# Kernel optimization log

Hardware: AMD Instinct MI355X
Metric: run time of the kernel (lower is better)

Reference implementation:

```python
import jax, jax.numpy as jnp
import numpy as np
from jax import lax

DIM, HEADS, BS, TOPK, WIN = 256, 8, 8, 4, 7
HID = 2 * DIM  # DBFFN ffn_expansion_factor=2
B, H, W = 2, 56, 56


def _lin(x, w, b=None):
    # torch Linear: y = x @ W.T + b, W is [out, in]
    y = jnp.einsum('...c,oc->...o', x, w)
    return y if b is None else y + b


def _ln(x, w, b, eps=1e-6):
    mu = jnp.mean(x, -1, keepdims=True)
    var = jnp.mean((x - mu) ** 2, -1, keepdims=True)
    return (x - mu) * lax.rsqrt(var + eps) * w + b


def _mha(Q, K, V, wq_w, wq_b, wk_w, wk_b, wv_w, wv_b, p_w, p_b):
    # standard cross MHA: Q [B,Nq,C], K/V [B,Nk,C]
    Bq, Nq, C = Q.shape
    h, d = HEADS, C // HEADS
    scale = d ** -0.5
    q = _lin(Q, wq_w, wq_b).reshape(Bq, Nq, h, d)
    k = _lin(K, wk_w, wk_b).reshape(Bq, -1, h, d)
    v = _lin(V, wv_w, wv_b).reshape(Bq, -1, h, d)
    attn = jax.nn.softmax(jnp.einsum('bnhd,bmhd->bhnm', q, k) * scale, axis=-1)
    out = jnp.einsum('bhnm,bmhd->bnhd', attn, v).reshape(Bq, Nq, C)
    return _lin(out, p_w, p_b)


def setup_inputs() -> dict:
    key = jax.random.key(0)
    ks = jax.random.split(key, 16)
    s = 0.02
    C = DIM
    inp = {
        'x': jax.random.normal(ks[0], (B, C, H, W), jnp.float32),
        'pos_w': jax.random.normal(ks[1], (C, 1, 3, 3), jnp.float32) * s,
        'pos_b': jnp.zeros((C,), jnp.float32),
        'n1_w': jnp.ones((C,), jnp.float32), 'n1_b': jnp.zeros((C,), jnp.float32),
        'n2_w': jnp.ones((C,), jnp.float32), 'n2_b': jnp.zeros((C,), jnp.float32),
        'wq_w': jax.random.normal(ks[2], (3, C, C), jnp.float32) * s,
        'wq_b': jnp.zeros((3, C), jnp.float32),
        'wk_w': jax.random.normal(ks[3], (3, C, C), jnp.float32) * s,
        'wk_b': jnp.zeros((3, C), jnp.float32),
        'wv_w': jax.random.normal(ks[4], (3, C, C), jnp.float32) * s,
        'wv_b': jnp.zeros((3, C), jnp.float32),
        'pj_w': jax.random.normal(ks[5], (3, C, C), jnp.float32) * s,
        'pj_b': jnp.zeros((3, C), jnp.float32),
        # block scorer
        's1_w': jax.random.normal(ks[6], (C // 2, C), jnp.float32) * s,
        's1_b': jnp.zeros((C // 2,), jnp.float32),
        's2_w': jax.random.normal(ks[7], (1, C // 2), jnp.float32) * s,
        's2_b': jnp.zeros((1,), jnp.float32),
        # gating: per-token softmax weights over 3 branches
        'g_w': jax.random.normal(ks[8], (3, C), jnp.float32) * s,
        'g_b': jnp.zeros((3,), jnp.float32),
        # DBFFN (gated dconv FFN, bias=False): in-proj C->2*HID, dw 3x3, out-proj HID->C
        'pin_w': jax.random.normal(ks[9], (2 * HID, C), jnp.float32) * s,
        'dw_w': jax.random.normal(ks[10], (3, 3, 1, 2 * HID), jnp.float32) * s,
        'pout_w': jax.random.normal(ks[11], (C, HID), jnp.float32) * s,
    }
    return inp


def _forward(x, pos_w, pos_b, n1_w, n1_b, n2_w, n2_b, wq_w, wq_b, wk_w, wk_b,
             wv_w, wv_b, pj_w, pj_b, s1_w, s1_b, s2_w, s2_b, g_w, g_b,
             pin_w, dw_w, pout_w):
    Bx, C, Hx, Wx = x.shape
    # depthwise positional conv
    pos = lax.conv_general_dilated(x, pos_w, (1, 1), 'SAME',
                                   dimension_numbers=('NCHW', 'OIHW', 'NCHW'),
                                   feature_group_count=C)
    x = x + pos + pos_b[None, :, None, None] * 0 + pos_b[None, :, None, None]
    feat = jnp.transpose(x, (0, 2, 3, 1))  # NHWC
    Nq = Hx * Wx
    Q = feat.reshape(Bx, Nq, C)
    # block means
    nH, nW = Hx // BS, Wx // BS
    nB = nH * nW
    blk = feat.reshape(Bx, nH, BS, nW, BS, C).transpose(0, 1, 3, 2, 4, 5)
    blk = blk.reshape(Bx, nB, BS * BS, C).mean(axis=2)  # [B,nB,C]
    # block scores + top-k selection
    hsc = jax.nn.gelu(_lin(blk, s1_w, s1_b), approximate=False)
    scores = _lin(hsc, s2_w, s2_b)[..., 0]  # [B,nB]
    topk = min(TOPK, nB)
    _, idx = lax.top_k(scores, topk)
    K_sel = jnp.take_along_axis(blk, idx[:, :, None], axis=1)  # [B,topk,C]
    # compressed + selected branches
    y_cmp = _mha(Q, blk, blk, wq_w[0], wq_b[0], wk_w[0], wk_b[0], wv_w[0], wv_b[0], pj_w[0], pj_b[0])
    y_sel = _mha(Q, K_sel, K_sel, wq_w[1], wq_b[1], wk_w[1], wk_b[1], wv_w[1], wv_b[1], pj_w[1], pj_b[1])
    # local window branch (replicate-pad + unfold == shifted slices)
    pad = WIN // 2
    padded = jnp.pad(feat, ((0, 0), (pad, pad), (pad, pad), (0, 0)), mode='edge')
    patches = jnp.stack([padded[:, dy:dy + Hx, dx:dx + Wx, :]
                         for dy in range(WIN) for dx in range(WIN)], axis=3)
    patches = patches.reshape(Bx, Nq, WIN * WIN, C)  # [B,Nq,49,C]
    h, d = HEADS, C // HEADS
    scale = d ** -0.5
    q = _lin(Q, wq_w[2], wq_b[2]).reshape(Bx, Nq, h, d)
    k = _lin(patches, wk_w[2], wk_b[2]).reshape(Bx, Nq, WIN * WIN, h, d)
    v = _lin(patches, wv_w[2], wv_b[2]).reshape(Bx, Nq, WIN * WIN, h, d)
    attn = jax.nn.softmax(jnp.einsum('bnhd,bnwhd->bnhw', q, k) * scale, axis=-1)
    y_win = jnp.einsum('bnhw,bnwhd->bnhd', attn, v).reshape(Bx, Nq, C)
    y_win = _lin(y_win, pj_w[2], pj_b[2])
    # gated fusion + residual
    qn = _ln(Q, n1_w, n1_b)
    g = jax.nn.softmax(_lin(qn, g_w, g_b), axis=-1)  # [B,Nq,3]
    y = g[..., 0:1] * y_cmp + g[..., 1:2] * y_sel + g[..., 2:3] * y_win + Q
    ym = y.reshape(Bx, Hx, Wx, C)
    # DBFFN: gated depthwise-conv FFN (bias-free)
    t = _lin(ym, pin_w)  # [B,H,W,2*HID]
    t = lax.conv_general_dilated(t, dw_w, (1, 1), 'SAME',
                                 dimension_numbers=('NHWC', 'HWIO', 'NHWC'),
                                 feature_group_count=2 * HID)
    x1, x2 = jnp.split(t, 2, axis=-1)
    mlp = _lin(jax.nn.gelu(x1, approximate=False) * x2, pout_w)
    ym = _ln(ym + mlp, n2_w, n2_b)
    return jnp.transpose(ym, (0, 3, 1, 2))  # NCHW


def reference(x, pos_w, pos_b, n1_w, n1_b, n2_w, n2_b, wq_w, wq_b, wk_w, wk_b,
              wv_w, wv_b, pj_w, pj_b, s1_w, s1_b, s2_w, s2_b, g_w, g_b,
              pin_w, dw_w, pout_w):
    return _forward(x, pos_w, pos_b, n1_w, n1_b, n2_w, n2_b, wq_w, wq_b, wk_w,
                    wk_b, wv_w, wv_b, pj_w, pj_b, s1_w, s1_b, s2_w, s2_b,
                    g_w, g_b, pin_w, dw_w, pout_w)
```

## Files before the change

### kernel.cpp

```cpp
#include <hip/hip_runtime.h>

#define BATCH 2
#define CDIM 256
#define HEADS 8
#define HD 32
#define HH 56
#define WW 56
#define NQ 3136
#define NTOK 6272
#define NB 49
#define NTOPK 4
#define HID2 1024
#define HIDM 512
#define QSTRH 1280
#define ASTR 768

typedef short bf16x8 __attribute__((ext_vector_type(8)));
typedef float f32x4 __attribute__((ext_vector_type(4)));
typedef _Float16 h2 __attribute__((ext_vector_type(2)));
typedef _Float16 h4 __attribute__((ext_vector_type(4)));
struct __align__(16) h2x4 { h2 x, y, z, w; };

__device__ __forceinline__ float gelu_exact(float x) {
    return 0.5f * x * (1.f + erff(x * 0.70710678118654752f));
}

__device__ __forceinline__ short f2bf(float f) {
    union { float f; unsigned u; } v; v.f = f;
    unsigned r = v.u + 0x7FFFu + ((v.u >> 16) & 1u);
    return (short)(r >> 16);
}

__device__ __forceinline__ float fdot2h(h2 a, h2 b, float c) {
#if __has_builtin(__builtin_amdgcn_fdot2)
    return __builtin_amdgcn_fdot2(a, b, c, false);
#else
    return c + (float)a[0] * (float)b[0] + (float)a[1] * (float)b[1];
#endif
}

__device__ __forceinline__ void gld16(const void* gsrc, void* ldst) {
    __builtin_amdgcn_global_load_lds(
        (const __attribute__((address_space(1))) void*)gsrc,
        (__attribute__((address_space(3))) void*)ldst, 16, 0, 0);
}

__global__ __launch_bounds__(256) void k_init(
        const float* __restrict__ x, float* __restrict__ xT,
        const float* __restrict__ wq_w, const float* __restrict__ wk_w,
        const float* __restrict__ wv_w, const float* __restrict__ wq_b,
        const float* __restrict__ wk_b, const float* __restrict__ wv_b,
        const float* __restrict__ pj_w, const float* __restrict__ pin_w,
        const float* __restrict__ pout_w,
        short* __restrict__ Wc1, short* __restrict__ Wpj,
        short* __restrict__ Wpin, short* __restrict__ Wpout,
        float* __restrict__ bias1, float* __restrict__ Wkv0,
        float* __restrict__ bkv0, float* __restrict__ Wkv1,
        float* __restrict__ bkv1) {
    __shared__ float t[64][65];
    int bid = blockIdx.x;
    int tid = threadIdx.x;
    if (bid < 392) {
        int p0 = (bid % 49) * 64;
        int c0 = ((bid / 49) & 3) * 64;
        int b  = bid / 196;
        int pi = tid & 63, cj = tid >> 6;
        #pragma unroll
        for (int j = 0; j < 16; j++) {
            int c = cj * 16 + j;
            t[c][pi] = x[((size_t)(b * CDIM + c0 + c)) * NQ + p0 + pi];
        }
        __syncthreads();
        int ci = tid & 63, pj = tid >> 6;
        #pragma unroll
        for (int j = 0; j < 16; j++) {
            int p = pj * 16 + j;
            xT[((size_t)(b * NQ + p0 + p)) * CDIM + c0 + ci] = t[ci][p];
        }
        return;
    }
    int i = (bid - 392) * 256 + tid;
    if (i < 327680) {
        int r = i >> 8, k = i & 255, seg = r >> 8, n = r & 255;
        float v;
        if (seg == 0)      v = wq_w[n * 256 + k];
        else if (seg == 1) v = wq_w[65536 + n * 256 + k];
        else if (seg == 2) v = wq_w[131072 + n * 256 + k];
        else if (seg == 3) v = wk_w[131072 + n * 256 + k];
        else               v = wv_w[131072 + n * 256 + k];
        Wc1[i] = f2bf(v);
    } else if (i < 524288) {
        int j = i - 327680;
        int n = j / 768, tt = j % 768, br = tt >> 8, k = tt & 255;
        Wpj[j] = f2bf(pj_w[br * 65536 + n * 256 + k]);
    } else if (i < 786432) {
        int j = i - 524288;
        int r = j >> 8, k = j & 255;
        int o = (r & 3) * 256 + (r >> 2);
        Wpin[j] = f2bf(pin_w[o * 256 + k]);
    } else if (i < 917504) {
        int j = i - 786432;
        Wpout[j] = f2bf(pout_w[j]);
    } else if (i < 1048576) {
        int j = i - 917504;
        int r = j >> 8, k = j & 255;
        Wkv0[j] = (r < 256) ? wk_w[r * 256 + k] : wv_w[(r - 256) * 256 + k];
    } else if (i < 1179648) {
        int j = i - 1048576;
        int r = j >> 8, k = j & 255;
        Wkv1[j] = (r < 256) ? wk_w[65536 + r * 256 + k] : wv_w[65536 + (r - 256) * 256 + k];
    } else if (i < 1180928) {
        int j = i - 1179648;
        float v;
        if (j < 768)       v = wq_b[j];
        else if (j < 1024) v = wk_b[512 + (j - 768)];
        else               v = wv_b[512 + (j - 1024)];
        bias1[j] = v;
    } else if (i < 1181440) {
        int j = i - 1180928;
        bkv0[j] = (j < 256) ? wk_b[j] : wv_b[j - 256];
    } else if (i < 1181952) {
        int j = i - 1181440;
        bkv1[j] = (j < 256) ? wk_b[256 + j] : wv_b[j];
    }
}

__global__ __launch_bounds__(256) void k_posgates(
        const float* __restrict__ xT, const float* __restrict__ pw,
        const float* __restrict__ pb, const float* __restrict__ n1w,
        const float* __restrict__ n1b, const float* __restrict__ gw,
        const float* __restrict__ gb, float* __restrict__ feat,
        float* __restrict__ g, short* __restrict__ featb) {
    int wvid = threadIdx.x >> 6;
    int lane = threadIdx.x & 63;
    int c4 = lane * 4;
    float pwv[4][9];
    #pragma unroll
    for (int j = 0; j < 4; j++)
        #pragma unroll
        for (int i = 0; i < 9; i++) pwv[j][i] = pw[(c4 + j) * 9 + i];
    float4 pbv = *(const float4*)(pb + c4);
    float4 w1 = *(const float4*)(n1w + c4);
    float4 b1 = *(const float4*)(n1b + c4);
    float4 gw0 = *(const float4*)(gw + c4);
    float4 gw1 = *(const float4*)(gw + CDIM + c4);
    float4 gw2 = *(const float4*)(gw + 2 * CDIM + c4);
    float gb0 = gb[0], gb1 = gb[1], gb2 = gb[2];
    int tbase = blockIdx.x * 16 + wvid * 4;
    for (int t = 0; t < 4; t++) {
        int bn = tbase + t;
        int b = bn / NQ, n = bn % NQ;
        int y = n / WW, x = n % WW;
        const float* xb = xT + (size_t)b * NQ * CDIM;
        float4 a = *(const float4*)(xb + (size_t)n * CDIM + c4);
        float acc0 = a.x + pbv.x, acc1 = a.y + pbv.y;
        float acc2 = a.z + pbv.z, acc3 = a.w + pbv.w;
        #pragma unroll
        for (int dy = 0; dy < 3; dy++) {
            int yy = y + dy - 1;
            if (yy < 0 || yy >= HH) continue;
            #pragma unroll
            for (int dx = 0; dx < 3; dx++) {
                int xx = x + dx - 1;
                if (xx < 0 || xx >= WW) continue;
                float4 v = *(const float4*)(xb + ((size_t)(yy * WW + xx)) * CDIM + c4);
                int wi = dy * 3 + dx;
                acc0 += v.x * pwv[0][wi];
                acc1 += v.y * pwv[1][wi];
                acc2 += v.z * pwv[2][wi];
                acc3 += v.w * pwv[3][wi];
            }
        }
        *(float4*)(feat + (size_t)bn * CDIM + c4) = make_float4(acc0, acc1, acc2, acc3);
        short4 fb;
        fb.x = f2bf(acc0); fb.y = f2bf(acc1); fb.z = f2bf(acc2); fb.w = f2bf(acc3);
        *(short4*)(featb + (size_t)bn * CDIM + c4) = fb;
        float s = acc0 + acc1 + acc2 + acc3;
        #pragma unroll
        for (int off = 32; off > 0; off >>= 1) s += __shfl_xor(s, off);
        float mu = s * (1.f / CDIM);
        float d0 = acc0 - mu, d1 = acc1 - mu, d2 = acc2 - mu, d3 = acc3 - mu;
        float ss = d0 * d0 + d1 * d1 + d2 * d2 + d3 * d3;
        #pragma unroll
        for (int off = 32; off > 0; off >>= 1) ss += __shfl_xor(ss, off);
        float rstd = rsqrtf(ss * (1.f / CDIM) + 1e-6f);
        float q0 = d0 * rstd * w1.x + b1.x;
        float q1 = d1 * rstd * w1.y + b1.y;
        float q2 = d2 * rstd * w1.z + b1.z;
        float q3 = d3 * rstd * w1.w + b1.w;
        float p0 = q0 * gw0.x + q1 * gw0.y + q2 * gw0.z + q3 * gw0.w;
        float p1 = q0 * gw1.x + q1 * gw1.y + q2 * gw1.z + q3 * gw1.w;
        float p2 = q0 * gw2.x + q1 * gw2.y + q2 * gw2.z + q3 * gw2.w;
        #pragma unroll
        for (int off = 32; off > 0; off >>= 1) {
            p0 += __shfl_xor(p0, off);
            p1 += __shfl_xor(p1, off);
            p2 += __shfl_xor(p2, off);
        }
        if (lane == 0) {
            float l0 = p0 + gb0, l1 = p1 + gb1, l2 = p2 + gb2;
            float m3 = fmaxf(l0, fmaxf(l1, l2));
            float e0 = __expf(l0 - m3), e1 = __expf(l1 - m3), e2 = __expf(l2 - m3);
            float inv = 1.f / (e0 + e1 + e2);
            g[bn * 3 + 0] = e0 * inv;
            g[bn * 3 + 1] = e1 * inv;
            g[bn * 3 + 2] = e2 * inv;
        }
    }
}

__global__ __launch_bounds__(256) void k_blkscore(
        const float* __restrict__ feat, const float* __restrict__ s1w,
        const float* __restrict__ s1b, const float* __restrict__ s2w,
        const float* __restrict__ s2b, float* __restrict__ blk,
        float* __restrict__ scores) {
    __shared__ float sblk[256];
    __shared__ float red[128];
    int gid = blockIdx.x;
    int b = gid / NB, bid = gid % NB;
    int by = bid / 7, bx = bid % 7;
    int c = threadIdx.x;
    float s = 0.f;
    for (int iy = 0; iy < 8; iy++)
        for (int ix = 0; ix < 8; ix++) {
            int y = by * 8 + iy, xx = bx * 8 + ix;
            s += feat[((size_t)(b * NQ + y * WW + xx)) * CDIM + c];
        }
    s *= (1.f / 64.f);
    blk[(size_t)gid * CDIM + c] = s;
    sblk[c] = s;
    __syncthreads();
    if (c < 128) {
        const float* wrow = s1w + (size_t)c * CDIM;
        float acc = s1b[c];
        for (int k = 0; k < CDIM; k++) acc += sblk[k] * wrow[k];
        red[c] = gelu_exact(acc) * s2w[c];
    }
    __syncthreads();
    #pragma unroll
    for (int st = 64; st > 0; st >>= 1) {
        if (c < st) red[c] += red[c + st];
        __syncthreads();
    }
    if (c == 0) scores[gid] = red[0] + s2b[0];
}

__global__ __launch_bounds__(256) void k_qkvkv(
        const short* __restrict__ A, const short* __restrict__ W,
        const float* __restrict__ bias, _Float16* __restrict__ C2,
        const float* __restrict__ blk, const float* __restrict__ Wkv0,
        const float* __restrict__ bkv0, _Float16* __restrict__ kvcmp,
        const float* __restrict__ scores, const float* __restrict__ Wkv1,
        const float* __restrict__ bkv1, _Float16* __restrict__ kvsel) {
    __shared__ __align__(16) char sm[27648];
    int bid = blockIdx.x;
    int tid = threadIdx.x;
    if (bid < 980) {
        const int K = 256, N = 1280;
        short (*As)[72] = (short(*)[72])sm;
        short (*Bs)[72] = (short(*)[72])(sm + 64 * 72 * 2);
        int wid = tid >> 6, lane = tid & 63;
        int wm = wid >> 1, wn = wid & 1;
        int m0 = (bid / 10) * 64, n0 = (bid % 10) * 128;
        f32x4 acc[2][4] = {};
        int ar = tid >> 2, ac = (tid & 3) * 16;
        int br = tid >> 1, bc = (tid & 1) * 32;
        int fr = lane & 15, fk = (lane >> 4) * 8;
        for (int k0 = 0; k0 < K; k0 += 64) {
            const short* ap = A + (size_t)(m0 + ar) * K + k0 + ac;
            bf16x8 a0 = *(const bf16x8*)(ap);
            bf16x8 a1 = *(const bf16x8*)(ap + 8);
            const short* wp = W + (size_t)(n0 + br) * K + k0 + bc;
            bf16x8 w0 = *(const bf16x8*)(wp);
            bf16x8 w1 = *(const bf16x8*)(wp + 8);
            bf16x8 w2 = *(const bf16x8*)(wp + 16);
            bf16x8 w3 = *(const bf16x8*)(wp + 24);
            __syncthreads();
            *(bf16x8*)&As[ar][ac] = a0;
            *(bf16x8*)&As[ar][ac + 8] = a1;
            *(bf16x8*)&Bs[br][bc] = w0;
            *(bf16x8*)&Bs[br][bc + 8] = w1;
            *(bf16x8*)&Bs[br][bc + 16] = w2;
            *(bf16x8*)&Bs[br][bc + 24] = w3;
            __syncthreads();
            #pragma unroll
            for (int kk = 0; kk < 64; kk += 32) {
                bf16x8 af[2], bf[4];
                #pragma unroll
                for (int mi = 0; mi < 2; mi++)
                    af[mi] = *(const bf16x8*)&As[wm * 32 + mi * 16 + fr][kk + fk];
                #pragma unroll
                for (int ni = 0; ni < 4; ni++)
                    bf[ni] = *(const bf16x8*)&Bs[wn * 64 + ni * 16 + fr][kk + fk];
                #pragma unroll
                for (int mi = 0; mi < 2; mi++)
                    #pragma unroll
                    for (int ni = 0; ni < 4; ni++)
                        acc[mi][ni] = __builtin_amdgcn_mfma_f32_16x16x32_bf16(
                            af[mi], bf[ni], acc[mi][ni], 0, 0, 0);
            }
        }
        int rsub = (lane >> 4) * 4;
        #pragma unroll
        for (int mi = 0; mi < 2; mi++) {
            #pragma unroll
            for (int ni = 0; ni < 4; ni++) {
                int col = n0 + wn * 64 + ni * 16 + (lane & 15);
                float bv = bias[col];
                #pragma unroll
                for (int r = 0; r < 4; r++) {
                    int row = m0 + wm * 32 + mi * 16 + rsub + r;
                    C2[(size_t)row * N + col] = (_Float16)(acc[mi][ni][r] + bv);
                }
            }
        }
    } else {
        float (*As)[68] = (float(*)[68])sm;
        float (*Ws)[68] = (float(*)[68])(sm + 16 * 68 * 4);
        float (*ssc)[NB] = (float(*)[NB])(sm + 2 * 16 * 68 * 4);
        int* sidx = (int*)(sm + 2 * 16 * 68 * 4 + 2 * NB * 4);
        int kid = bid - 980;
        int kvy = kid >> 3, kvx = kid & 7;
        const float* Wk; const float* biask; _Float16* C; int M;
        int m0;
        bool sel = (kvy == 2);
        if (!sel) { Wk = Wkv0; biask = bkv0; C = kvcmp; M = 98; m0 = kvy * 64; }
        else      { Wk = Wkv1; biask = bkv1; C = kvsel; M = 8;  m0 = 0; }
        const int N = 512, K = 256;
        const int tx = tid & 15, ty = tid >> 4;
        const int n0 = kvx * 64;
        const int lr = tid >> 2;
        const int lk = (tid & 3) * 4;
        if (sel) {
            if (tid < 2 * NB) ssc[tid / NB][tid % NB] = scores[tid];
            __syncthreads();
            if (tid < 2) {
                for (int t = 0; t < NTOPK; t++) {
                    int best = 0; float bv = -1e30f;
                    for (int m = 0; m < NB; m++)
                        if (ssc[tid][m] > bv) { bv = ssc[tid][m]; best = m; }
                    sidx[tid * 4 + t] = best; ssc[tid][best] = -1e30f;
                }
            }
            __syncthreads();
        }
        int gm = m0 + lr;
        int arow = gm;
        if (sel && gm < 8) arow = (gm >> 2) * NB + sidx[gm];
        float acc[4][4] = {};
        for (int k0 = 0; k0 < K; k0 += 16) {
            float4 av = make_float4(0.f, 0.f, 0.f, 0.f);
            if (gm < M) av = *(const float4*)(blk + (size_t)arow * K + k0 + lk);
            int gn = n0 + lr;
            float4 wv = *(const float4*)(Wk + (size_t)gn * K + k0 + lk);
            __syncthreads();
            As[lk][lr] = av.x; As[lk + 1][lr] = av.y; As[lk + 2][lr] = av.z; As[lk + 3][lr] = av.w;
            Ws[lk][lr] = wv.x; Ws[lk + 1][lr] = wv.y; Ws[lk + 2][lr] = wv.z; Ws[lk + 3][lr] = wv.w;
            __syncthreads();
            #pragma unroll
            for (int kk = 0; kk < 16; kk++) {
                const float4 a = *(const float4*)&As[kk][ty * 4];
                const float4 b = *(const float4*)&Ws[kk][tx * 4];
                acc[0][0] += a.x * b.x; acc[0][1] += a.x * b.y; acc[0][2] += a.x * b.z; acc[0][3] += a.x * b.w;
                acc[1][0] += a.y * b.x; acc[1][1] += a.y * b.y; acc[1][2] += a.y * b.z; acc[1][3] += a.y * b.w;
                acc[2][0] += a.z * b.x; acc[2][1] += a.z * b.y; acc[2][2] += a.z * b.z; acc[2][3] += a.z * b.w;
                acc[3][0] += a.w * b.x; acc[3][1] += a.w * b.y; acc[3][2] += a.w * b.z; acc[3][3] += a.w * b.w;
            }
        }
        #pragma unroll
        for (int i = 0; i < 4; i++) {
            int om = m0 + ty * 4 + i;
            if (om >= M) break;
            #pragma unroll
            for (int j = 0; j < 4; j++) {
                int gn = n0 + tx * 4 + j;
                C[(size_t)om * N + gn] = (_Float16)(acc[i][j] + biask[gn]);
            }
        }
    }
}

__global__ __launch_bounds__(256) void k_gemm64x128(
        const short* __restrict__ A, const short* __restrict__ W,
        const float* __restrict__ bias, int M, int N, int K,
        _Float16* __restrict__ C2) {
    __shared__ short As[64][72];
    __shared__ short Bs[128][72];
    int tid = threadIdx.x;
    int wid = tid >> 6, lane = tid & 63;
    int wm = wid >> 1, wn = wid & 1;
    int m0 = blockIdx.y * 64, n0 = blockIdx.x * 128;
    f32x4 acc[2][4] = {};
    int ar = tid >> 2, ac = (tid & 3) * 16;
    int br = tid >> 1, bc = (tid & 1) * 32;
    int fr = lane & 15, fk = (lane >> 4) * 8;
    for (int k0 = 0; k0 < K; k0 += 64) {
        const short* ap = A + (size_t)(m0 + ar) * K + k0 + ac;
        bf16x8 a0 = *(const bf16x8*)(ap);
        bf16x8 a1 = *(const bf16x8*)(ap + 8);
        const short* wp = W + (size_t)(n0 + br) * K + k0 + bc;
        bf16x8 w0 = *(const bf16x8*)(wp);
        bf16x8 w1 = *(const bf16x8*)(wp + 8);
        bf16x8 w2 = *(const bf16x8*)(wp + 16);
        bf16x8 w3 = *(const bf16x8*)(wp + 24);
        __syncthreads();
        *(bf16x8*)&As[ar][ac] = a0;
        *(bf16x8*)&As[ar][ac + 8] = a1;
        *(bf16x8*)&Bs[br][bc] = w0;
        *(bf16x8*)&Bs[br][bc + 8] = w1;
        *(bf16x8*)&Bs[br][bc + 16] = w2;
        *(bf16x8*)&Bs[br][bc + 24] = w3;
        __syncthreads();
        #pragma unroll
        for (int kk = 0; kk < 64; kk += 32) {
            bf16x8 af[2], bf[4];
            #pragma unroll
            for (int mi = 0; mi < 2; mi++)
                af[mi] = *(const bf16x8*)&As[wm * 32 + mi * 16 + fr][kk + fk];
            #pragma unroll
            for (int ni = 0; ni < 4; ni++)
                bf[ni] = *(const bf16x8*)&Bs[wn * 64 + ni * 16 + fr][kk + fk];
            #pragma unroll
            for (int mi = 0; mi < 2; mi++)
                #pragma unroll
                for (int ni = 0; ni < 4; ni++)
                    acc[mi][ni] = __builtin_amdgcn_mfma_f32_16x16x32_bf16(
                        af[mi], bf[ni], acc[mi][ni], 0, 0, 0);
        }
    }
    int rsub = (lane >> 4) * 4;
    #pragma unroll
    for (int mi = 0; mi < 2; mi++) {
        #pragma unroll
        for (int ni = 0; ni < 4; ni++) {
            int col = n0 + wn * 64 + ni * 16 + (lane & 15);
            float bv = bias ? bias[col] : 0.f;
            #pragma unroll
            for (int r = 0; r < 4; r++) {
                int row = m0 + wm * 32 + mi * 16 + rsub + r;
                C2[(size_t)row * N + col] = (_Float16)(acc[mi][ni][r] + bv);
            }
        }
    }
}

__global__ __launch_bounds__(256) void k_gemm64(
        const short* __restrict__ A, const short* __restrict__ W,
        const float* __restrict__ bias, float* __restrict__ C,
        int M, int N, int K,
        const float* __restrict__ resid, const float* __restrict__ g3,
        const float* __restrict__ pjb, short* __restrict__ Cb) {
    __shared__ short As[64][72];
    __shared__ short Bs[64][72];
    int tid = threadIdx.x;
    int wid = tid >> 6, lane = tid & 63;
    int wm = wid >> 1, wn = wid & 1;
    int m0 = blockIdx.y * 64, n0 = blockIdx.x * 64;
    f32x4 acc[2][2] = {};
    int ar = tid >> 2, ac = (tid & 3) * 16;
    int fr = lane & 15, fk = (lane >> 4) * 8;
    for (int k0 = 0; k0 < K; k0 += 64) {
        const short* ap = A + (size_t)(m0 + ar) * K + k0 + ac;
        bf16x8 a0 = *(const bf16x8*)(ap);
        bf16x8 a1 = *(const bf16x8*)(ap + 8);
        const short* wp = W + (size_t)(n0 + ar) * K + k0 + ac;
        bf16x8 w0 = *(const bf16x8*)(wp);
        bf16x8 w1 = *(const bf16x8*)(wp + 8);
        __syncthreads();
        *(bf16x8*)&As[ar][ac] = a0;
        *(bf16x8*)&As[ar][ac + 8] = a1;
        *(bf16x8*)&Bs[ar][ac] = w0;
        *(bf16x8*)&Bs[ar][ac + 8] = w1;
        __syncthreads();
        #pragma unroll
        for (int kk = 0; kk < 64; kk += 32) {
            bf16x8 af[2], bf[2];
            #pragma unroll
            for (int mi = 0; mi < 2; mi++)
                af[mi] = *(const bf16x8*)&As[wm * 32 + mi * 16 + fr][kk + fk];
            #pragma unroll
            for (int ni = 0; ni < 2; ni++)
                bf[ni] = *(const bf16x8*)&Bs[wn * 32 + ni * 16 + fr][kk + fk];
            #pragma unroll
            for (int mi = 0; mi < 2; mi++)
                #pragma unroll
                for (int ni = 0; ni < 2; ni++)
                    acc[mi][ni] = __builtin_amdgcn_mfma_f32_16x16x32_bf16(
                        af[mi], bf[ni], acc[mi][ni], 0, 0, 0);
        }
    }
    int rsub = (lane >> 4) * 4;
    #pragma unroll
    for (int mi = 0; mi < 2; mi++) {
        #pragma unroll
        for (int ni = 0; ni < 2; ni++) {
            int col = n0 + wn * 32 + ni * 16 + (lane & 15);
            #pragma unroll
            for (int r = 0; r < 4; r++) {
                int row = m0 + wm * 32 + mi * 16 + rsub + r;
                float v = acc[mi][ni][r];
                if (resid) {
                    v += resid[(size_t)row * N + col]
                       + g3[row * 3 + 0] * pjb[col]
                       + g3[row * 3 + 1] * pjb[256 + col]
                       + g3[row * 3 + 2] * pjb[512 + col];
                } else if (bias) {
                    v += bias[col];
                }
                C[(size_t)row * N + col] = v;
                if (Cb) Cb[(size_t)row * N + col] = f2bf(v);
            }
        }
    }
}

__global__ __launch_bounds__(256) void k_poutln(
        const short* __restrict__ G, const short* __restrict__ W,
        const float* __restrict__ ym, const float* __restrict__ n2w,
        const float* __restrict__ n2b, float* __restrict__ out) {
    __shared__ short As[32][72];
    __shared__ float redS[4][36];
    __shared__ float redQ[4][36];
    int tid = threadIdx.x;
    int wid = tid >> 6, lane = tid & 63;
    int bx = blockIdx.x;
    int b = bx / 98;
    int t0g = bx * 32;
    int p0 = (bx % 98) * 32;
    f32x4 acc[2][4] = {};
    int ar = tid >> 3, ac = (tid & 7) * 8;
    int fr = lane & 15, fk = (lane >> 4) * 8;
    const short* Wb = W + (size_t)(wid * 64) * 512;
    for (int k0 = 0; k0 < 512; k0 += 64) {
        bf16x8 a0 = *(const bf16x8*)(G + (size_t)(t0g + ar) * 512 + k0 + ac);
        __syncthreads();
        *(bf16x8*)&As[ar][ac] = a0;
        __syncthreads();
        #pragma unroll
        for (int kk = 0; kk < 64; kk += 32) {
            bf16x8 af[2], bf[4];
            #pragma unroll
            for (int mi = 0; mi < 2; mi++)
                af[mi] = *(const bf16x8*)&As[mi * 16 + fr][kk + fk];
            #pragma unroll
            for (int ni = 0; ni < 4; ni++)
                bf[ni] = *(const bf16x8*)(Wb + (size_t)(ni * 16 + fr) * 512 + k0 + kk + fk);
            #pragma unroll
            for (int mi = 0; mi < 2; mi++)
                #pragma unroll
                for (int ni = 0; ni < 4; ni++)
                    acc[mi][ni] = __builtin_amdgcn_mfma_f32_16x16x32_bf16(
                        af[mi], bf[ni], acc[mi][ni], 0, 0, 0);
        }
    }
    int rsub = (lane >> 4) * 4;
    float v[2][4][4];
    #pragma unroll
    for (int mi = 0; mi < 2; mi++)
        #pragma unroll
        for (int ni = 0; ni < 4; ni++) {
            int col = wid * 64 + ni * 16 + fr;
            #pragma unroll
            for (int r = 0; r < 4; r++) {
                int row = mi * 16 + rsub + r;
                v[mi][ni][r] = acc[mi][ni][r] + ym[(size_t)(t0g + row) * CDIM + col];
            }
        }
    #pragma unroll
    for (int mi = 0; mi < 2; mi++) {
        #pragma unroll
        for (int r = 0; r < 4; r++) {
            float s = v[mi][0][r] + v[mi][1][r] + v[mi][2][r] + v[mi][3][r];
            s += __shfl_xor(s, 1); s += __shfl_xor(s, 2);
            s += __shfl_xor(s, 4); s += __shfl_xor(s, 8);
            if (fr == 0) redS[wid][mi * 16 + rsub + r] = s;
        }
    }
    __syncthreads();
    float mu[2][4];
    #pragma unroll
    for (int mi = 0; mi < 2; mi++)
        #pragma unroll
        for (int r = 0; r < 4; r++) {
            int row = mi * 16 + rsub + r;
            mu[mi][r] = (redS[0][row] + redS[1][row] + redS[2][row] + redS[3][row])
                        * (1.f / CDIM);
        }
    #pragma unroll
    for (int mi = 0; mi < 2; mi++) {
        #pragma unroll
        for (int r = 0; r < 4; r++) {
            float m = mu[mi][r];
            float d0 = v[mi][0][r] - m, d1 = v[mi][1][r] - m;
            float d2 = v[mi][2][r] - m, d3 = v[mi][3][r] - m;
            float q = d0 * d0 + d1 * d1 + d2 * d2 + d3 * d3;
            q += __shfl_xor(q, 1); q += __shfl_xor(q, 2);
            q += __shfl_xor(q, 4); q += __shfl_xor(q, 8);
            if (fr == 0) redQ[wid][mi * 16 + rsub + r] = q;
        }
    }
    __syncthreads();
    float rstd[2][4];
    #pragma unroll
    for (int mi = 0; mi < 2; mi++)
        #pragma unroll
        for (int r = 0; r < 4; r++) {
            int row = mi * 16 + rsub + r;
            float var = (redQ[0][row] + redQ[1][row] + redQ[2][row] + redQ[3][row])
                        * (1.f / CDIM);
            rstd[mi][r] = rsqrtf(var + 1e-6f);
        }
    #pragma unroll
    for (int mi = 0; mi < 2; mi++) {
        #pragma unroll
        for (int ni = 0; ni < 4; ni++) {
            int col = wid * 64 + ni * 16 + fr;
            float wgt = n2w[col], bia = n2b[col];
            float4 o;
            o.x = (v[mi][ni][0] - mu[mi][0]) * rstd[mi][0] * wgt + bia;
            o.y = (v[mi][ni][1] - mu[mi][1]) * rstd[mi][1] * wgt + bia;
            o.z = (v[mi][ni][2] - mu[mi][2]) * rstd[mi][2] * wgt + bia;
            o.w = (v[mi][ni][3] - mu[mi][3]) * rstd[mi][3] * wgt + bia;
            *(float4*)(out + ((size_t)(b * CDIM + col)) * NQ + p0 + mi * 16 + rsub) = o;
        }
    }
}

__global__ __launch_bounds__(512) void k_attn_lds(
        const _Float16* __restrict__ bufQ, const _Float16* __restrict__ kvc,
        const _Float16* __restrict__ kvs, short* __restrict__ Acatb,
        const float* __restrict__ g) {
    __shared__ uint4 buf[100 * 32];
    int tid = threadIdx.x;
    int wid = tid >> 6;
    int lane = tid & 63;
    int l = tid & 31;
    int tk = tid >> 5;
    int dg = l & 3;
    int co = l * 8;
    const float scale = 0.17677669529663687f;

    if (blockIdx.x < 392) {
        int bid = blockIdx.x;
        int swz = (bid & 7) * 49 + (bid >> 3);
        int t0 = swz * 16;
        int tok = t0 + tk;
        int b = t0 / NQ;
        const _Float16* kb = kvc + (size_t)b * NB * 512;
        for (int p = wid * 2; p < NB + 1; p += 16) {
            int myp = p + (lane >> 5);
            if (myp > NB - 1) myp = NB - 1;
            gld16((const uint4*)(kb + (size_t)myp * 512) + (lane & 31), &buf[p * 32]);
        }
        const _Float16* qrow = bufQ + (size_t)tok * QSTRH;
        float gate0 = g[tok * 3 + 0];
        float gate1 = g[tok * 3 + 1];
        short* orow = Acatb + (size_t)tok * ASTR;
        h2x4 qv = *(const h2x4*)(qrow + co);
        __syncthreads();
        float sc[13];
        sc[12] = -1e30f;
        #pragma unroll
        for (int m = 0; m < NB; m++) {
            h2x4 kv = *(const h2x4*)&buf[m * 32 + l];
            float acc = fdot2h(qv.x, kv.x, 0.f);
            acc = fdot2h(qv.y, kv.y, acc);
            acc = fdot2h(qv.z, kv.z, acc);
            acc = fdot2h(qv.w, kv.w, acc);
            acc += __shfl_xor(acc, 1);
            acc += __shfl_xor(acc, 2);
            if ((m & 3) == dg) sc[m >> 2] = acc * scale;
        }
        float mx = sc[0];
        #pragma unroll
        for (int i = 1; i < 13; i++) mx = fmaxf(mx, sc[i]);
        mx = fmaxf(mx, __shfl_xor(mx, 1));
        mx = fmaxf(mx, __shfl_xor(mx, 2));
        float sum = 0.f;
        #pragma unroll
        for (int i = 0; i < 13; i++) { sc[i] = __expf(sc[i] - mx); sum += sc[i]; }
        sum += __shfl_xor(sum, 1);
        sum += __shfl_xor(sum, 2);
        float inv_c = 1.f / sum;
        __syncthreads();
        for (int p = wid * 2; p < NB + 1; p += 16) {
            int myp = p + (lane >> 5);
            if (myp > NB - 1) myp = NB - 1;
            gld16((const uint4*)(kb + (size_t)myp * 512 + 256) + (lane & 31), &buf[p * 32]);
        }
        {
            const _Float16* ksb = kvs + (size_t)b * NTOPK * 512;
            h2x4 qs = *(const h2x4*)(qrow + 256 + co);
            float sv = 0.f;
            #pragma unroll
            for (int m = 0; m < NTOPK; m++) {
                h2x4 kk = *(const h2x4*)(ksb + (size_t)m * 512 + co);
                float acc = fdot2h(qs.x, kk.x, 0.f);
                acc = fdot2h(qs.y, kk.y, acc);
                acc = fdot2h(qs.z, kk.z, acc);
                acc = fdot2h(qs.w, kk.w, acc);
                acc += __shfl_xor(acc, 1);
                acc += __shfl_xor(acc, 2);
                if (m == dg) sv = acc * scale;
            }
            float mxs = sv;
            mxs = fmaxf(mxs, __shfl_xor(mxs, 1));
            mxs = fmaxf(mxs, __shfl_xor(mxs, 2));
            float e = __expf(sv - mxs);
            float sums = e;
            sums += __shfl_xor(sums, 1);
            sums += __shfl_xor(sums, 2);
            float invs = 1.f / sums;
            float o[8];
            #pragma unroll
            for (int d = 0; d < 8; d++) o[d] = 0.f;
            #pragma unroll
            for (int m = 0; m < NTOPK; m++) {
                float pw = __shfl(e, m, 4);
                h2x4 vv = *(const h2x4*)(ksb + (size_t)m * 512 + 256 + co);
                o[0] += pw * (float)vv.x[0]; o[1] += pw * (float)vv.x[1];
                o[2] += pw * (float)vv.y[0]; o[3] += pw * (float)vv.y[1];
                o[4] += pw * (float)vv.z[0]; o[5] += pw * (float)vv.z[1];
                o[6] += pw * (float)vv.w[0]; o[7] += pw * (float)vv.w[1];
            }
            float gg = gate1 * invs;
            bf16x8 ov;
            #pragma unroll
            for (int d = 0; d < 8; d++) ov[d] = f2bf(o[d] * gg);
            *(bf16x8*)(orow + 256 + co) = ov;
        }
        __syncthreads();
        {
            float o[8];
            #pragma unroll
            for (int d = 0; d < 8; d++) o[d] = 0.f;
            #pragma unroll
            for (int m = 0; m < NB; m++) {
                float pw = __shfl(sc[m >> 2], m & 3, 4);
                h2x4 vv = *(const h2x4*)&buf[m * 32 + l];
                o[0] += pw * (float)vv.x[0]; o[1] += pw * (float)vv.x[1];
                o[2] += pw * (float)vv.y[0]; o[3] += pw * (float)vv.y[1];
                o[4] += pw * (float)vv.z[0]; o[5] += pw * (float)vv.z[1];
                o[6] += pw * (float)vv.w[0]; o[7] += pw * (float)vv.w[1];
            }
            float gg = gate0 * inv_c;
            bf16x8 ov;
            #pragma unroll
            for (int d = 0; d < 8; d++) ov[d] = f2bf(o[d] * gg);
            *(bf16x8*)(orow + co) = ov;
        }
    } else {
        int bid = blockIdx.x - 392;
        int swz = (bid & 7) * 49 + (bid >> 3);
        int b = swz / 196;
        int r = swz % 196;
        int y0 = (r / 14) * 4;
        int x0 = (r % 14) * 4;
        int ty = tk >> 2, tx = tk & 3;
        int y = y0 + ty, x = x0 + tx;
        int tok = b * NQ + y * WW + x;
        const _Float16* KVb = bufQ + (size_t)b * NQ * QSTRH;
        for (int p = wid * 2; p < 100; p += 16) {
            int pp = p + (lane >> 5);
            int pr = pp / 10, pc = pp - pr * 10;
            int gy = min(max(y0 + pr - 3, 0), HH - 1);
            int gx = min(max(x0 + pc - 3, 0), WW - 1);
            gld16((const uint4*)(KVb + (size_t)(gy * WW + gx) * QSTRH + 768) + (lane & 31),
                  &buf[p * 32]);
        }
        h2x4 qv = *(const h2x4*)(bufQ + (size_t)tok * QSTRH + 512 + co);
        float gate = g[tok * 3 + 2];
        __syncthreads();
        float sw[13];
        sw[12] = -1e30f;
        #pragma unroll
        for (int dy = 0; dy < 7; dy++) {
            #pragma unroll
            for (int dx = 0; dx < 7; dx++) {
                int p = (ty + dy) * 10 + tx + dx;
                h2x4 kv = *(const h2x4*)&buf[p * 32 + l];
                float acc = fdot2h(qv.x, kv.x, 0.f);
                acc = fdot2h(qv.y, kv.y, acc);
                acc = fdot2h(qv.z, kv.z, acc);
                acc = fdot2h(qv.w, kv.w, acc);
                acc += __shfl_xor(acc, 1);
                acc += __shfl_xor(acc, 2);
                int m = dy * 7 + dx;
                if ((m & 3) == dg) sw[m >> 2] = acc * scale;
            }
        }
        float mx = sw[0];
        #pragma unroll
        for (int i = 1; i < 13; i++) mx = fmaxf(mx, sw[i]);
        mx = fmaxf(mx, __shfl_xor(mx, 1));
        mx = fmaxf(mx, __shfl_xor(mx, 2));
        float sum = 0.f;
        #pragma unroll
        for (int i = 0; i < 13; i++) { sw[i] = __expf(sw[i] - mx); sum += sw[i]; }
        sum += __shfl_xor(sum, 1);
        sum += __shfl_xor(sum, 2);
        float inv = 1.f / sum;
        __syncthreads();
        for (int p = wid * 2; p < 100; p += 16) {
            int pp = p + (lane >> 5);
            int pr = pp / 10, pc = pp - pr * 10;
            int gy = min(max(y0 + pr - 3, 0), HH - 1);
            int gx = min(max(x0 + pc - 3, 0), WW - 1);
            gld16((const uint4*)(KVb + (size_t)(gy * WW + gx) * QSTRH + 1024) + (lane & 31),
                  &buf[p * 32]);
        }
        __syncthreads();
        float o[8];
        #pragma unroll
        for (int d = 0; d < 8; d++) o[d] = 0.f;
        #pragma unroll
        for (int dy = 0; dy < 7; dy++) {
            #pragma unroll
            for (int dx = 0; dx < 7; dx++) {
                int p = (ty + dy) * 10 + tx + dx;
                int m = dy * 7 + dx;
                float pw = __shfl(sw[m >> 2], m & 3, 4);
                h2x4 vv = *(const h2x4*)&buf[p * 32 + l];
                o[0] += pw * (float)vv.x[0]; o[1] += pw * (float)vv.x[1];
                o[2] += pw * (float)vv.y[0]; o[3] += pw * (float)vv.y[1];
                o[4] += pw * (float)vv.z[0]; o[5] += pw * (float)vv.z[1];
                o[6] += pw * (float)vv.w[0]; o[7] += pw * (float)vv.w[1];
            }
        }
        float gg = gate * inv;
        short* op = Acatb + (size_t)tok * ASTR + 512 + co;
        bf16x8 ov;
        #pragma unroll
        for (int d = 0; d < 8; d++) ov[d] = f2bf(o[d] * gg);
        *(bf16x8*)(op) = ov;
    }
}

__global__ __launch_bounds__(256) void k_dwglu2(
        const _Float16* __restrict__ t, const float* __restrict__ w,
        short* __restrict__ G) {
    int gid = blockIdx.x;
    int xq = gid & 7;
    int y0 = ((gid >> 3) % (HH / 2)) * 2;
    int b = gid / ((HH / 2) * 8);
    int c = threadIdx.x;
    float wv[9][4];
    #pragma unroll
    for (int i = 0; i < 9; i++)
        #pragma unroll
        for (int j = 0; j < 4; j++) wv[i][j] = w[i * HID2 + j * 256 + c];
    const _Float16* tb = t + (size_t)b * NQ * HID2;
    short* Gbase = G + (size_t)b * NQ * HIDM;
    int x0 = xq * 7;
    float col[3][4][4];
    #pragma unroll
    for (int ci = 0; ci < 2; ci++) {
        int xx = x0 - 1 + ci;
        #pragma unroll
        for (int r = 0; r < 4; r++) {
            int yy = y0 + r - 1;
            bool ok = (xx >= 0) && (yy >= 0) && (yy < HH);
            h4 v = {};
            if (ok) v = *(const h4*)(tb + ((size_t)(yy * WW + xx)) * HID2 + c * 4);
            #pragma unroll
            for (int j = 0; j < 4; j++) col[ci][r][j] = (float)v[j];
        }
    }
    #pragma unroll
    for (int i = 0; i < 7; i++) {
        int xx = x0 + i;
        {
            int xl = xx + 1;
            #pragma unroll
            for (int r = 0; r < 4; r++) {
                int yy = y0 + r - 1;
                bool ok = (xl < WW) && (yy >= 0) && (yy < HH);
                h4 v = {};
                if (ok) v = *(const h4*)(tb + ((size_t)(yy * WW + xl)) * HID2 + c * 4);
                #pragma unroll
                for (int j = 0; j < 4; j++) col[(i + 2) % 3][r][j] = (float)v[j];
            }
        }
        #pragma unroll
        for (int o = 0; o < 2; o++) {
            float a0 = 0.f, a1 = 0.f, a2 = 0.f, a3 = 0.f;
            #pragma unroll
            for (int r = 0; r < 3; r++) {
                #pragma unroll
                for (int dxx = 0; dxx < 3; dxx++) {
                    const float* cc = col[(i + dxx) % 3][r + o];
                    int wi = r * 3 + dxx;
                    a0 += cc[0] * wv[wi][0];
                    a1 += cc[1] * wv[wi][1];
                    a2 += cc[2] * wv[wi][2];
                    a3 += cc[3] * wv[wi][3];
                }
            }
            short* Gb = Gbase + (size_t)((y0 + o) * WW + xx) * HIDM;
            Gb[c]       = f2bf(gelu_exact(a0) * a2);
            Gb[c + 256] = f2bf(gelu_exact(a1) * a3);
        }
    }
}

extern "C" void kernel_launch(void* const* d_in, const int* in_sizes, int n_in,
                              void* d_out, int out_size, void* d_ws, size_t ws_size,
                              hipStream_t stream) {
    const float* x     = (const float*)d_in[0];
    const float* pos_w = (const float*)d_in[1];
    const float* pos_b = (const float*)d_in[2];
    const float* n1w   = (const float*)d_in[3];
    const float* n1b   = (const float*)d_in[4];
    const float* n2w   = (const float*)d_in[5];
    const float* n2b   = (const float*)d_in[6];
    const float* wq_w  = (const float*)d_in[7];
    const float* wq_b  = (const float*)d_in[8];
    const float* wk_w  = (const float*)d_in[9];
    const float* wk_b  = (const float*)d_in[10];
    const float* wv_w  = (const float*)d_in[11];
    const float* wv_b  = (const float*)d_in[12];
    const float* pj_w  = (const float*)d_in[13];
    const float* pj_b  = (const float*)d_in[14];
    const float* s1w   = (const float*)d_in[15];
    const float* s1b   = (const float*)d_in[16];
    const float* s2w   = (const float*)d_in[17];
    const float* s2b   = (const float*)d_in[18];
    const float* gw    = (const float*)d_in[19];
    const float* gb    = (const float*)d_in[20];
    const float* pinw  = (const float*)d_in[21];
    const float* dww   = (const float*)d_in[22];
    const float* poutw = (const float*)d_in[23];
    float* out = (float*)d_out;
    float* ws  = (float*)d_ws;

    const size_t SZ = (size_t)NTOK * CDIM;
    float* feat = ws;
    _Float16* bufQh = (_Float16*)(feat + SZ);
    float* R1   = (float*)(bufQh + (size_t)NTOK * QSTRH);
    float* xT   = R1;
    short* Acatb = (short*)R1;
    _Float16* T1h = (_Float16*)R1;
    float* ym   = R1 + (size_t)NTOK * 512;
    short* featb = (short*)(ym + SZ);
    short* ymb   = featb + (size_t)NTOK * CDIM;
    float* blk   = (float*)(ymb + (size_t)NTOK * CDIM);
    _Float16* kvcmp = (_Float16*)(blk + 98 * 256);
    _Float16* kvsel = kvcmp + 98 * 512;
    float* scores = (float*)(kvsel + 8 * 512);
    float* g      = scores + 128;
    float* bias1  = g + (size_t)NTOK * 3;
    float* Wkv0   = bias1 + 1280;
    float* bkv0   = Wkv0 + 512 * 256;
    float* Wkv1   = bkv0 + 512;
    float* bkv1   = Wkv1 + 512 * 256;
    short* Wc1    = (short*)(bkv1 + 512);
    short* Wpj    = Wc1 + 1280 * 256;
    short* Wpin   = Wpj + 256 * 768;
    short* Wpout  = Wpin + 1024 * 256;
    short* G      = (short*)bufQh;

    hipLaunchKernelGGL(k_init, dim3(392 + 4618), dim3(256), 0, stream,
                       x, xT, wq_w, wk_w, wv_w, wq_b, wk_b, wv_b, pj_w, pinw, poutw,
                       Wc1, Wpj, Wpin, Wpout, bias1, Wkv0, bkv0, Wkv1, bkv1);
    hipLaunchKernelGGL(k_posgates, dim3(NTOK / 16), dim3(256), 0, stream,
                       xT, pos_w, pos_b, n1w, n1b, gw, gb, feat, g, featb);
    hipLaunchKernelGGL(k_blkscore, dim3(BATCH * NB), dim3(256), 0, stream,
                       feat, s1w, s1b, s2w, s2b, blk, scores);
    hipLaunchKernelGGL(k_qkvkv, dim3(1004), dim3(256), 0, stream,
                       featb, Wc1, bias1, bufQh,
                       blk, Wkv0, bkv0, kvcmp, scores, Wkv1, bkv1, kvsel);
    hipLaunchKernelGGL(k_attn_lds, dim3(784), dim3(512), 0, stream,
                       bufQh, kvcmp, kvsel, Acatb, g);
    hipLaunchKernelGGL(k_gemm64, dim3(CDIM / 64, NTOK / 64), dim3(256), 0, stream,
                       Acatb, Wpj, nullptr, ym, NTOK, CDIM, ASTR, feat, g, pj_b, ymb);
    hipLaunchKernelGGL(k_gemm64x128, dim3(HID2 / 128, NTOK / 64), dim3(256), 0, stream,
                       ymb, Wpin, nullptr, NTOK, HID2, 256, T1h);
    hipLaunchKernelGGL(k_dwglu2, dim3(BATCH * (HH / 2) * 8), dim3(256), 0, stream, T1h, dww, G);
    hipLaunchKernelGGL(k_poutln, dim3(NTOK / 32), dim3(256), 0, stream,
                       G, Wpout, ym, n2w, n2b, out);
}
```

Measured before the change: 157.7 us.

## Store transposed input as fp16 and swizzle GEMM blocks across XCDs

The transposed input buffer is now stored in fp16 instead of fp32, which halves the bytes written by the init transpose and read by the depthwise positional conv. The three GEMM kernels remap block indices so that consecutive tiles land on the same XCD, with the aim of improving L2 reuse of the shared A and B tiles on the chiplet-based GPU. The fp16 input adds rounding error to the positional-conv input. The swizzle in the grid GEMMs assumes the block count divides evenly by 8.

```diff
diff --git a/kernel.cpp b/kernel.cpp
--- a/kernel.cpp
+++ b/kernel.cpp
@@ -46,7 +46,7 @@
 }
 
 __global__ __launch_bounds__(256) void k_init(
-        const float* __restrict__ x, float* __restrict__ xT,
+        const float* __restrict__ x, _Float16* __restrict__ xTh,
         const float* __restrict__ wq_w, const float* __restrict__ wk_w,
         const float* __restrict__ wv_w, const float* __restrict__ wq_b,
         const float* __restrict__ wk_b, const float* __restrict__ wv_b,
@@ -75,7 +75,7 @@
         #pragma unroll
         for (int j = 0; j < 16; j++) {
             int p = pj * 16 + j;
-            xT[((size_t)(b * NQ + p0 + p)) * CDIM + c0 + ci] = t[ci][p];
+            xTh[((size_t)(b * NQ + p0 + p)) * CDIM + c0 + ci] = (_Float16)t[ci][p];
         }
         return;
     }
@@ -126,7 +126,7 @@
 }
 
 __global__ __launch_bounds__(256) void k_posgates(
-        const float* __restrict__ xT, const float* __restrict__ pw,
+        const _Float16* __restrict__ xTh, const float* __restrict__ pw,
         const float* __restrict__ pb, const float* __restrict__ n1w,
         const float* __restrict__ n1b, const float* __restrict__ gw,
         const float* __restrict__ gb, float* __restrict__ feat,
@@ -151,10 +151,10 @@
         int bn = tbase + t;
         int b = bn / NQ, n = bn % NQ;
         int y = n / WW, x = n % WW;
-        const float* xb = xT + (size_t)b * NQ * CDIM;
-        float4 a = *(const float4*)(xb + (size_t)n * CDIM + c4);
-        float acc0 = a.x + pbv.x, acc1 = a.y + pbv.y;
-        float acc2 = a.z + pbv.z, acc3 = a.w + pbv.w;
+        const _Float16* xb = xTh + (size_t)b * NQ * CDIM;
+        h4 a = *(const h4*)(xb + (size_t)n * CDIM + c4);
+        float acc0 = (float)a[0] + pbv.x, acc1 = (float)a[1] + pbv.y;
+        float acc2 = (float)a[2] + pbv.z, acc3 = (float)a[3] + pbv.w;
         #pragma unroll
         for (int dy = 0; dy < 3; dy++) {
             int yy = y + dy - 1;
@@ -163,12 +163,12 @@
             for (int dx = 0; dx < 3; dx++) {
                 int xx = x + dx - 1;
                 if (xx < 0 || xx >= WW) continue;
-                float4 v = *(const float4*)(xb + ((size_t)(yy * WW + xx)) * CDIM + c4);
+                h4 v = *(const h4*)(xb + ((size_t)(yy * WW + xx)) * CDIM + c4);
                 int wi = dy * 3 + dx;
-                acc0 += v.x * pwv[0][wi];
-                acc1 += v.y * pwv[1][wi];
-                acc2 += v.z * pwv[2][wi];
-                acc3 += v.w * pwv[3][wi];
+                acc0 += (float)v[0] * pwv[0][wi];
+                acc1 += (float)v[1] * pwv[1][wi];
+                acc2 += (float)v[2] * pwv[2][wi];
+                acc3 += (float)v[3] * pwv[3][wi];
             }
         }
         *(float4*)(feat + (size_t)bn * CDIM + c4) = make_float4(acc0, acc1, acc2, acc3);
@@ -256,12 +256,14 @@
     int bid = blockIdx.x;
     int tid = threadIdx.x;
     if (bid < 980) {
+        int xcd = bid & 7, idx = bid >> 3;
+        int swb = (xcd < 4) ? xcd * 123 + idx : 492 + (xcd - 4) * 122 + idx;
         const int K = 256, N = 1280;
         short (*As)[72] = (short(*)[72])sm;
         short (*Bs)[72] = (short(*)[72])(sm + 64 * 72 * 2);
         int wid = tid >> 6, lane = tid & 63;
         int wm = wid >> 1, wn = wid & 1;
-        int m0 = (bid / 10) * 64, n0 = (bid % 10) * 128;
+        int m0 = (swb / 10) * 64, n0 = (swb % 10) * 128;
         f32x4 acc[2][4] = {};
         int ar = tid >> 2, ac = (tid & 3) * 16;
         int br = tid >> 1, bc = (tid & 1) * 32;
@@ -389,7 +391,10 @@
     int tid = threadIdx.x;
     int wid = tid >> 6, lane = tid & 63;
     int wm = wid >> 1, wn = wid & 1;
-    int m0 = blockIdx.y * 64, n0 = blockIdx.x * 128;
+    int lin = blockIdx.y * gridDim.x + blockIdx.x;
+    int cpx = (gridDim.x * gridDim.y) >> 3;
+    int swz = (lin & 7) * cpx + (lin >> 3);
+    int m0 = (swz / gridDim.x) * 64, n0 = (swz % gridDim.x) * 128;
     f32x4 acc[2][4] = {};
     int ar = tid >> 2, ac = (tid & 3) * 16;
     int br = tid >> 1, bc = (tid & 1) * 32;
@@ -455,7 +460,10 @@
     int tid = threadIdx.x;
     int wid = tid >> 6, lane = tid & 63;
     int wm = wid >> 1, wn = wid & 1;
-    int m0 = blockIdx.y * 64, n0 = blockIdx.x * 64;
+    int lin = blockIdx.y * gridDim.x + blockIdx.x;
+    int cpx = (gridDim.x * gridDim.y) >> 3;
+    int swz = (lin & 7) * cpx + (lin >> 3);
+    int m0 = (swz / gridDim.x) * 64, n0 = (swz % gridDim.x) * 64;
     f32x4 acc[2][2] = {};
     int ar = tid >> 2, ac = (tid & 3) * 16;
     int fr = lane & 15, fk = (lane >> 4) * 8;
@@ -937,7 +945,7 @@
     float* feat = ws;
     _Float16* bufQh = (_Float16*)(feat + SZ);
     float* R1   = (float*)(bufQh + (size_t)NTOK * QSTRH);
-    float* xT   = R1;
+    _Float16* xTh = (_Float16*)R1;
     short* Acatb = (short*)R1;
     _Float16* T1h = (_Float16*)R1;
     float* ym   = R1 + (size_t)NTOK * 512;
@@ -960,10 +968,10 @@
     short* G      = (short*)bufQh;
 
     hipLaunchKernelGGL(k_init, dim3(392 + 4618), dim3(256), 0, stream,
-                       x, xT, wq_w, wk_w, wv_w, wq_b, wk_b, wv_b, pj_w, pinw, poutw,
+                       x, xTh, wq_w, wk_w, wv_w, wq_b, wk_b, wv_b, pj_w, pinw, poutw,
                        Wc1, Wpj, Wpin, Wpout, bias1, Wkv0, bkv0, Wkv1, bkv1);
     hipLaunchKernelGGL(k_posgates, dim3(NTOK / 16), dim3(256), 0, stream,
-                       xT, pos_w, pos_b, n1w, n1b, gw, gb, feat, g, featb);
+                       xTh, pos_w, pos_b, n1w, n1b, gw, gb, feat, g, featb);
     hipLaunchKernelGGL(k_blkscore, dim3(BATCH * NB), dim3(256), 0, stream,
                        feat, s1w, s1b, s2w, s2b, blk, scores);
     hipLaunchKernelGGL(k_qkvkv, dim3(1004), dim3(256), 0, stream,
```

New measurement: 159.0 us. No clear change (+0.8%).
